# Optimization experiments

Measured on AMD Instinct MI355X. Metric: run time of the kernel, lower is better.

## Reference

```python
import jax, jax.numpy as jnp
import numpy as np

D_MODEL = 256
N_HEADS = 8
WS = 4          # window size
SHIFTED = True
HEAD_DIM = D_MODEL // N_HEADS


def _shift_masks(ws):
    # Masks for the last row / last column of windows after the cyclic shift
    # (standard from-scratch Swin shifted-window mask construction).
    T = ws * ws
    s = ws * (ws // 2)
    row = np.zeros((T, T), np.float32)
    row[-s:, :-s] = -np.inf
    row[:-s, -s:] = -np.inf
    # einops '(r w1) (c w2) -> (w1 r) (w2 c)' with w1=w2=ws
    col = row.reshape(ws, ws, ws, ws).transpose(1, 0, 3, 2).reshape(T, T)
    return jnp.asarray(row), jnp.asarray(col)


def setup_inputs() -> dict:
    key = jax.random.key(0)
    kx, kw, kb = jax.random.split(key, 3)
    x = jax.random.normal(kx, (32, 56 * 56, D_MODEL), jnp.float32)
    W = jax.random.normal(kw, (D_MODEL, 3 * D_MODEL), jnp.float32) * 0.02
    b = jax.random.normal(kb, (3 * D_MODEL,), jnp.float32) * 0.02
    return {"x": x, "W": W, "b": b}


def reference(x, W, b):
    B, L, D = x.shape
    h = w = int(np.sqrt(L))
    ws, nh, hd = WS, N_HEADS, HEAD_DIM
    # QKV projection; torch code splits last dim as (heads, head_dim, 3) -> K innermost
    qkv = (x @ W + b).reshape(B, h, w, nh, hd, 3)
    if SHIFTED:
        qkv = jnp.roll(qkv, (-(ws // 2), -(ws // 2)), axis=(1, 2))
    nwh, nww = h // ws, w // ws
    # window partition: b (i m1) (j m2) n e k -> b n i j (m1 m2) e k
    qkv = qkv.reshape(B, nwh, ws, nww, ws, nh, hd, 3)
    qkv = qkv.transpose(0, 5, 1, 3, 2, 4, 6, 7).reshape(B, nh, nwh, nww, ws * ws, hd, 3)
    q, k, v = qkv[..., 0], qkv[..., 1], qkv[..., 2]
    scores = jnp.einsum('bnijte,bnijse->bnijts', q, k) / jnp.sqrt(jnp.float32(hd))
    if SHIFTED:
        row_mask, col_mask = _shift_masks(ws)
        scores = scores.at[:, :, -1, :].add(row_mask)   # last row of windows
        scores = scores.at[:, :, :, -1].add(col_mask)   # last column of windows
    att = jax.nn.softmax(scores, axis=-1)
    out = jnp.einsum('bnijts,bnijse->bnijte', att, v)
    # reverse window partition: b n i j (m1 m2) e -> b (i m1) (j m2) (n e)
    out = out.reshape(B, nh, nwh, nww, ws, ws, hd)
    out = out.transpose(0, 2, 4, 3, 5, 1, 6).reshape(B, h, w, D)
    if SHIFTED:
        out = jnp.roll(out, (ws // 2, ws // 2), axis=(1, 2))
    return out.reshape(B, L, D)
```

## Files before the change

kernel.cpp:

```cpp
#include <hip/hip_runtime.h>

typedef __attribute__((ext_vector_type(8))) short short8;
typedef __attribute__((ext_vector_type(4))) short short4v;
typedef __attribute__((ext_vector_type(4))) float floatx4;

#define NWSIDE 14
#define HLEN   56
#define DM     256

#define QK_STRIDE 264
#define K_OFF     4224
#define VT_OFF    4224
#define WINB      8448

static __device__ __forceinline__ unsigned int f2bfu(float f) {
    unsigned int u = __float_as_uint(f);
    return (u + 0x7fffu + ((u >> 16) & 1u)) >> 16;
}
static __device__ __forceinline__ unsigned short f2bf(float f) {
    return (unsigned short)f2bfu(f);
}

__global__ void swin_prep(const float* __restrict__ W, const float* __restrict__ bias,
                          unsigned short* __restrict__ Wt, float* __restrict__ bperm) {
    const int k = blockIdx.x;
    const int ks = k >> 5, lq = (k >> 3) & 3, j = k & 7;
    #pragma unroll
    for (int it = 0; it < 3; ++it) {
        const int c = it * 256 + threadIdx.x;
        const float w = W[(size_t)k * 768 + c];
        const int h = c / 96, r = c - h * 96;
        const int e = r / 3, sect = r - e * 3;
        const int cp = h * 96 + sect * 32 + e;
        const int t = cp >> 4, lrow = cp & 15;
        Wt[(size_t)(((t * 8 + ks) * 64 + lq * 16 + lrow) << 3) + j] = f2bf(w);
        if (k == 0) bperm[cp] = bias[c];
    }
}

__global__ __launch_bounds__(256, 4)
void swin_mfma(const float* __restrict__ x,
               const unsigned short* __restrict__ Wt,
               const float* __restrict__ bperm,
               float* __restrict__ out) {
    __shared__ __align__(16) unsigned short lds[2 * WINB];

    const int b    = blockIdx.x / 98;
    const int g    = blockIdx.x % 98;
    const int tid  = threadIdx.x;
    const int wv   = tid >> 6;
    const int lane = tid & 63;
    const int lrow = lane & 15;
    const int lq   = lane >> 4;
    const float scale = 0.17677669529663687f;
    const floatx4 zf = {0.f, 0.f, 0.f, 0.f};

    const int u2 = tid >> 7, tk = (tid >> 3) & 15, sg = tid & 7;
    const int ww2 = g * 2 + u2;
    const int wi2 = ww2 / NWSIDE, wj2 = ww2 % NWSIDE;
    const int gr2 = (wi2 * 4 + (tk >> 2) + 2) % HLEN;
    const int gc2 = (wj2 * 4 + (tk & 3) + 2) % HLEN;
    const size_t rowoff = ((size_t)(b * 3136 + gr2 * 56 + gc2)) * DM;

    {
        const floatx4* xr = (const floatx4*)(x + rowoff);
        unsigned short* xd = &lds[u2 * WINB + tk * QK_STRIDE];
        #pragma unroll
        for (int j = 0; j < 8; ++j) {
            floatx4 f = xr[sg + 8 * j];
            short4v p;
            p[0] = (short)f2bf(f[0]); p[1] = (short)f2bf(f[1]);
            p[2] = (short)f2bf(f[2]); p[3] = (short)f2bf(f[3]);
            *(short4v*)&xd[(sg + 8 * j) * 4] = p;
        }
    }
    __syncthreads();

    const unsigned short* wbase = Wt + (size_t)(96 * wv) * 512 + (size_t)(lane * 8);

    short8 Ab[4];
    #pragma unroll
    for (int f = 0; f < 4; ++f)
        Ab[f] = *(const short8*)(wbase + (f << 9));

    short8 xf[2][8];
    #pragma unroll
    for (int u = 0; u < 2; ++u)
        #pragma unroll
        for (int ks = 0; ks < 8; ++ks)
            xf[u][ks] = *(const short8*)&lds[u * WINB + lrow * QK_STRIDE + ks * 32 + lq * 8];
    __syncthreads();

    floatx4 acc0, acc1, bcv;
    #pragma unroll
    for (int f = 0; f < 64; ++f) {
        const int pi = f >> 3, ks = f & 7;
        if (ks == 0) {
            const int t = 12 * wv + 6 * (pi >> 2) + (pi & 3);
            bcv = *(const floatx4*)&bperm[t * 16 + lq * 4];
            acc0 = zf; acc1 = zf;
        }
        const short8 a = Ab[f & 3];
        if (f + 4 < 64) {
            const int pn = (f + 4) >> 3, kn = (f + 4) & 7;
            Ab[f & 3] = *(const short8*)(wbase + ((48 * (pn >> 2) + 8 * (pn & 3) + kn) << 9));
        }
        acc0 = __builtin_amdgcn_mfma_f32_16x16x32_bf16(a, xf[0][ks], acc0, 0, 0, 0);
        acc1 = __builtin_amdgcn_mfma_f32_16x16x32_bf16(a, xf[1][ks], acc1, 0, 0, 0);
        if (ks == 7) {
            const int h    = 2 * wv + (pi >> 2);
            const int sect = (pi >> 1) & 1;
            const int e0   = (pi & 1) * 16;
            const int base = (sect ? K_OFF : 0) + lrow * QK_STRIDE + h * 32 + e0 + lq * 4;
            short4v p0, p1;
            p0[0] = (short)f2bf(acc0[0] + bcv[0]); p0[1] = (short)f2bf(acc0[1] + bcv[1]);
            p0[2] = (short)f2bf(acc0[2] + bcv[2]); p0[3] = (short)f2bf(acc0[3] + bcv[3]);
            p1[0] = (short)f2bf(acc1[0] + bcv[0]); p1[1] = (short)f2bf(acc1[1] + bcv[1]);
            p1[2] = (short)f2bf(acc1[2] + bcv[2]); p1[3] = (short)f2bf(acc1[3] + bcv[3]);
            *(short4v*)&lds[base]        = p0;
            *(short4v*)&lds[WINB + base] = p1;
        }
    }

    #pragma unroll
    for (int f = 0; f < 4; ++f)
        Ab[f] = *(const short8*)(wbase + ((32 + f) << 9));
    __syncthreads();

    const int u     = wv >> 1;
    const int hbase = (wv & 1) * 4;
    const int ww = g * 2 + u;
    const int wi = ww / NWSIDE, wj = ww % NWSIDE;
    const bool lastrow = (wi == NWSIDE - 1);
    const bool lastcol = (wj == NWSIDE - 1);
    const unsigned short* wl = lds + u * WINB;
    const bool mrow = lastrow && ((lrow >= 8) != (lq >= 2));
    const bool mc   = ((lrow & 3) >= 2);
    const int vtq = (lq & 1) * 8;

    floatx4 ST[4];
    #pragma unroll
    for (int hh = 0; hh < 4; ++hh) {
        const int h = hbase + hh;
        short8 Ak = *(const short8*)&wl[K_OFF + lrow * QK_STRIDE + h * 32 + lq * 8];
        short8 Bq = *(const short8*)&wl[lrow * QK_STRIDE + h * 32 + lq * 8];
        ST[hh] = __builtin_amdgcn_mfma_f32_16x16x32_bf16(Ak, Bq, zf, 0, 0, 0);
    }
    __syncthreads();

    #pragma unroll
    for (int f = 0; f < 32; ++f) {
        const int pi = f >> 3, ks = f & 7;
        if (ks == 0) {
            const int t = 12 * wv + 6 * (pi >> 1) + 4 + (pi & 1);
            bcv = *(const floatx4*)&bperm[t * 16 + lq * 4];
            acc0 = zf; acc1 = zf;
        }
        const short8 a = Ab[f & 3];
        if (f + 4 < 32) {
            const int pn = (f + 4) >> 3, kn = (f + 4) & 7;
            Ab[f & 3] = *(const short8*)(wbase + ((48 * (pn >> 1) + 32 + 8 * (pn & 1) + kn) << 9));
        }
        acc0 = __builtin_amdgcn_mfma_f32_16x16x32_bf16(a, xf[0][ks], acc0, 0, 0, 0);
        acc1 = __builtin_amdgcn_mfma_f32_16x16x32_bf16(a, xf[1][ks], acc1, 0, 0, 0);
        if (ks == 7) {
            const int h  = 2 * wv + (pi >> 1);
            const int e0 = (pi & 1) * 16;
            #pragma unroll
            for (int i = 0; i < 4; ++i) {
                const int rowe = h * 32 + e0 + lq * 4 + i;
                lds[VT_OFF + rowe * 16 + lrow]        = f2bf(acc0[i] + bcv[i]);
                lds[WINB + VT_OFF + rowe * 16 + lrow] = f2bf(acc1[i] + bcv[i]);
            }
        }
    }
    __syncthreads();

    const int gr5 = (wi * 4 + (lrow >> 2) + 2) % HLEN;
    const int gc5 = (wj * 4 + (lrow & 3) + 2) % HLEN;
    float* op = out + ((size_t)(b * 3136 + gr5 * 56 + gc5)) * DM;

    #pragma unroll
    for (int hh = 0; hh < 4; ++hh) {
        const int h = hbase + hh;
        float ev[4];
        #pragma unroll
        for (int i = 0; i < 4; ++i) {
            bool m = mrow || (lastcol && (mc != (i >= 2)));
            ev[i] = __expf(m ? -1e30f : ST[hh][i] * scale);
        }
        float rs = (ev[0] + ev[1]) + (ev[2] + ev[3]);
        rs += __shfl_xor(rs, 16);
        rs += __shfl_xor(rs, 32);
        const float inv = 1.0f / rs;
        const unsigned int d0 = f2bfu(ev[0] * inv) | (f2bfu(ev[1] * inv) << 16);
        const unsigned int d1 = f2bfu(ev[2] * inv) | (f2bfu(ev[3] * inv) << 16);
        const int src0 = lrow + ((lq & 1) << 5);
        int b0 = __shfl((int)d0, src0);
        int b1 = __shfl((int)d1, src0);
        int b2 = __shfl((int)d0, src0 + 16);
        int b3 = __shfl((int)d1, src0 + 16);
        if (lq >= 2) { b0 = 0; b1 = 0; b2 = 0; b3 = 0; }
        union { int i4[4]; short8 s8; } bp;
        bp.i4[0] = b0; bp.i4[1] = b1; bp.i4[2] = b2; bp.i4[3] = b3;
        #pragma unroll
        for (int eb = 0; eb < 2; ++eb) {
            short8 Av = *(const short8*)&wl[VT_OFF + (h * 32 + eb * 16 + lrow) * 16 + vtq];
            floatx4 O = __builtin_amdgcn_mfma_f32_16x16x32_bf16(Av, bp.s8, zf, 0, 0, 0);
            *(floatx4*)&op[h * 32 + eb * 16 + lq * 4] = O;
        }
    }
}

extern "C" void kernel_launch(void* const* d_in, const int* in_sizes, int n_in,
                              void* d_out, int out_size, void* d_ws, size_t ws_size,
                              hipStream_t stream) {
    const float* x    = (const float*)d_in[0];
    const float* W    = (const float*)d_in[1];
    const float* bias = (const float*)d_in[2];
    float* out = (float*)d_out;
    (void)in_sizes; (void)n_in; (void)out_size; (void)ws_size;

    unsigned short* Wt = (unsigned short*)d_ws;
    float* bperm = (float*)((char*)d_ws + 768 * 256 * 2);

    swin_prep<<<256, 256, 0, stream>>>(W, bias, Wt, bperm);
    swin_mfma<<<32 * 98, 256, 0, stream>>>(x, Wt, bperm, out);
}
```

Baseline: 256.9 us.

## Process four windows per block to amortize weight fragment loads across more MFMAs

Each block now handles four windows instead of two, so every weight fragment loaded from global memory feeds four MFMAs instead of two. This halves total weight traffic. The weight prefetch ring grows from four to eight fragments and runs continuously across the Q/K and V projection phases. In the attention phase each wave now handles all eight heads of one window instead of four heads of half a window. The cost is twice the LDS per block, more registers (xf[4][8], acc[4], ST[8]), launch bounds lowered to 2 blocks per CU, and half as many blocks in the grid.

```diff
diff --git a/kernel.cpp b/kernel.cpp
--- a/kernel.cpp
+++ b/kernel.cpp
@@ -19,6 +19,12 @@
 }
 static __device__ __forceinline__ unsigned short f2bf(float f) {
     return (unsigned short)f2bfu(f);
+}
+
+static __device__ __forceinline__ int wfrag_off(int G) {
+    if (G < 64) { const int pi = G >> 3, ks = G & 7; return 48 * (pi >> 2) + 8 * (pi & 3) + ks; }
+    const int Gb = G - 64, pi = Gb >> 3, ks = Gb & 7;
+    return 48 * (pi >> 1) + 32 + 8 * (pi & 1) + ks;
 }
 
 __global__ void swin_prep(const float* __restrict__ W, const float* __restrict__ bias,
@@ -38,15 +44,15 @@
     }
 }
 
-__global__ __launch_bounds__(256, 4)
+__global__ __launch_bounds__(256, 2)
 void swin_mfma(const float* __restrict__ x,
                const unsigned short* __restrict__ Wt,
                const float* __restrict__ bperm,
                float* __restrict__ out) {
-    __shared__ __align__(16) unsigned short lds[2 * WINB];
-
-    const int b    = blockIdx.x / 98;
-    const int g    = blockIdx.x % 98;
+    __shared__ __align__(16) unsigned short lds[4 * WINB];
+
+    const int b    = blockIdx.x / 49;
+    const int g    = blockIdx.x % 49;
     const int tid  = threadIdx.x;
     const int wv   = tid >> 6;
     const int lane = tid & 63;
@@ -55,8 +61,8 @@
     const float scale = 0.17677669529663687f;
     const floatx4 zf = {0.f, 0.f, 0.f, 0.f};
 
-    const int u2 = tid >> 7, tk = (tid >> 3) & 15, sg = tid & 7;
-    const int ww2 = g * 2 + u2;
+    const int tk = lane >> 2, sg = lane & 3;
+    const int ww2 = g * 4 + wv;
     const int wi2 = ww2 / NWSIDE, wj2 = ww2 % NWSIDE;
     const int gr2 = (wi2 * 4 + (tk >> 2) + 2) % HLEN;
     const int gc2 = (wj2 * 4 + (tk & 3) + 2) % HLEN;
@@ -64,87 +70,81 @@
 
     {
         const floatx4* xr = (const floatx4*)(x + rowoff);
-        unsigned short* xd = &lds[u2 * WINB + tk * QK_STRIDE];
-        #pragma unroll
-        for (int j = 0; j < 8; ++j) {
-            floatx4 f = xr[sg + 8 * j];
+        unsigned short* xd = &lds[wv * WINB + tk * QK_STRIDE];
+        #pragma unroll
+        for (int j = 0; j < 16; ++j) {
+            floatx4 f = xr[sg + 4 * j];
             short4v p;
             p[0] = (short)f2bf(f[0]); p[1] = (short)f2bf(f[1]);
             p[2] = (short)f2bf(f[2]); p[3] = (short)f2bf(f[3]);
-            *(short4v*)&xd[(sg + 8 * j) * 4] = p;
+            *(short4v*)&xd[(sg + 4 * j) * 4] = p;
         }
     }
     __syncthreads();
 
     const unsigned short* wbase = Wt + (size_t)(96 * wv) * 512 + (size_t)(lane * 8);
 
-    short8 Ab[4];
-    #pragma unroll
-    for (int f = 0; f < 4; ++f)
-        Ab[f] = *(const short8*)(wbase + (f << 9));
-
-    short8 xf[2][8];
-    #pragma unroll
-    for (int u = 0; u < 2; ++u)
+    short8 Ab[8];
+    #pragma unroll
+    for (int f = 0; f < 8; ++f)
+        Ab[f] = *(const short8*)(wbase + (wfrag_off(f) << 9));
+
+    short8 xf[4][8];
+    #pragma unroll
+    for (int u = 0; u < 4; ++u)
         #pragma unroll
         for (int ks = 0; ks < 8; ++ks)
             xf[u][ks] = *(const short8*)&lds[u * WINB + lrow * QK_STRIDE + ks * 32 + lq * 8];
     __syncthreads();
 
-    floatx4 acc0, acc1, bcv;
+    floatx4 acc[4], bcv;
     #pragma unroll
     for (int f = 0; f < 64; ++f) {
         const int pi = f >> 3, ks = f & 7;
         if (ks == 0) {
             const int t = 12 * wv + 6 * (pi >> 2) + (pi & 3);
             bcv = *(const floatx4*)&bperm[t * 16 + lq * 4];
-            acc0 = zf; acc1 = zf;
-        }
-        const short8 a = Ab[f & 3];
-        if (f + 4 < 64) {
-            const int pn = (f + 4) >> 3, kn = (f + 4) & 7;
-            Ab[f & 3] = *(const short8*)(wbase + ((48 * (pn >> 2) + 8 * (pn & 3) + kn) << 9));
-        }
-        acc0 = __builtin_amdgcn_mfma_f32_16x16x32_bf16(a, xf[0][ks], acc0, 0, 0, 0);
-        acc1 = __builtin_amdgcn_mfma_f32_16x16x32_bf16(a, xf[1][ks], acc1, 0, 0, 0);
+            #pragma unroll
+            for (int u = 0; u < 4; ++u) acc[u] = zf;
+        }
+        const short8 a = Ab[f & 7];
+        Ab[f & 7] = *(const short8*)(wbase + (wfrag_off(f + 8) << 9));
+        #pragma unroll
+        for (int u = 0; u < 4; ++u)
+            acc[u] = __builtin_amdgcn_mfma_f32_16x16x32_bf16(a, xf[u][ks], acc[u], 0, 0, 0);
         if (ks == 7) {
             const int h    = 2 * wv + (pi >> 2);
             const int sect = (pi >> 1) & 1;
             const int e0   = (pi & 1) * 16;
             const int base = (sect ? K_OFF : 0) + lrow * QK_STRIDE + h * 32 + e0 + lq * 4;
-            short4v p0, p1;
-            p0[0] = (short)f2bf(acc0[0] + bcv[0]); p0[1] = (short)f2bf(acc0[1] + bcv[1]);
-            p0[2] = (short)f2bf(acc0[2] + bcv[2]); p0[3] = (short)f2bf(acc0[3] + bcv[3]);
-            p1[0] = (short)f2bf(acc1[0] + bcv[0]); p1[1] = (short)f2bf(acc1[1] + bcv[1]);
-            p1[2] = (short)f2bf(acc1[2] + bcv[2]); p1[3] = (short)f2bf(acc1[3] + bcv[3]);
-            *(short4v*)&lds[base]        = p0;
-            *(short4v*)&lds[WINB + base] = p1;
-        }
-    }
-
-    #pragma unroll
-    for (int f = 0; f < 4; ++f)
-        Ab[f] = *(const short8*)(wbase + ((32 + f) << 9));
-    __syncthreads();
-
-    const int u     = wv >> 1;
-    const int hbase = (wv & 1) * 4;
-    const int ww = g * 2 + u;
+            #pragma unroll
+            for (int u = 0; u < 4; ++u) {
+                short4v p;
+                p[0] = (short)f2bf(acc[u][0] + bcv[0]);
+                p[1] = (short)f2bf(acc[u][1] + bcv[1]);
+                p[2] = (short)f2bf(acc[u][2] + bcv[2]);
+                p[3] = (short)f2bf(acc[u][3] + bcv[3]);
+                *(short4v*)&lds[u * WINB + base] = p;
+            }
+        }
+    }
+    __syncthreads();
+
+    const int ww = g * 4 + wv;
     const int wi = ww / NWSIDE, wj = ww % NWSIDE;
     const bool lastrow = (wi == NWSIDE - 1);
     const bool lastcol = (wj == NWSIDE - 1);
-    const unsigned short* wl = lds + u * WINB;
+    const unsigned short* wl = lds + wv * WINB;
     const bool mrow = lastrow && ((lrow >= 8) != (lq >= 2));
     const bool mc   = ((lrow & 3) >= 2);
     const int vtq = (lq & 1) * 8;
 
-    floatx4 ST[4];
-    #pragma unroll
-    for (int hh = 0; hh < 4; ++hh) {
-        const int h = hbase + hh;
+    floatx4 ST[8];
+    #pragma unroll
+    for (int h = 0; h < 8; ++h) {
         short8 Ak = *(const short8*)&wl[K_OFF + lrow * QK_STRIDE + h * 32 + lq * 8];
         short8 Bq = *(const short8*)&wl[lrow * QK_STRIDE + h * 32 + lq * 8];
-        ST[hh] = __builtin_amdgcn_mfma_f32_16x16x32_bf16(Ak, Bq, zf, 0, 0, 0);
+        ST[h] = __builtin_amdgcn_mfma_f32_16x16x32_bf16(Ak, Bq, zf, 0, 0, 0);
     }
     __syncthreads();
 
@@ -154,24 +154,25 @@
         if (ks == 0) {
             const int t = 12 * wv + 6 * (pi >> 1) + 4 + (pi & 1);
             bcv = *(const floatx4*)&bperm[t * 16 + lq * 4];
-            acc0 = zf; acc1 = zf;
-        }
-        const short8 a = Ab[f & 3];
-        if (f + 4 < 32) {
-            const int pn = (f + 4) >> 3, kn = (f + 4) & 7;
-            Ab[f & 3] = *(const short8*)(wbase + ((48 * (pn >> 1) + 32 + 8 * (pn & 1) + kn) << 9));
-        }
-        acc0 = __builtin_amdgcn_mfma_f32_16x16x32_bf16(a, xf[0][ks], acc0, 0, 0, 0);
-        acc1 = __builtin_amdgcn_mfma_f32_16x16x32_bf16(a, xf[1][ks], acc1, 0, 0, 0);
+            #pragma unroll
+            for (int u = 0; u < 4; ++u) acc[u] = zf;
+        }
+        const short8 a = Ab[f & 7];
+        if (f < 24)
+            Ab[f & 7] = *(const short8*)(wbase + (wfrag_off(72 + f) << 9));
+        #pragma unroll
+        for (int u = 0; u < 4; ++u)
+            acc[u] = __builtin_amdgcn_mfma_f32_16x16x32_bf16(a, xf[u][ks], acc[u], 0, 0, 0);
         if (ks == 7) {
             const int h  = 2 * wv + (pi >> 1);
             const int e0 = (pi & 1) * 16;
             #pragma unroll
-            for (int i = 0; i < 4; ++i) {
-                const int rowe = h * 32 + e0 + lq * 4 + i;
-                lds[VT_OFF + rowe * 16 + lrow]        = f2bf(acc0[i] + bcv[i]);
-                lds[WINB + VT_OFF + rowe * 16 + lrow] = f2bf(acc1[i] + bcv[i]);
-            }
+            for (int u = 0; u < 4; ++u)
+                #pragma unroll
+                for (int i = 0; i < 4; ++i) {
+                    const int rowe = h * 32 + e0 + lq * 4 + i;
+                    lds[u * WINB + VT_OFF + rowe * 16 + lrow] = f2bf(acc[u][i] + bcv[i]);
+                }
         }
     }
     __syncthreads();
@@ -181,13 +182,12 @@
     float* op = out + ((size_t)(b * 3136 + gr5 * 56 + gc5)) * DM;
 
     #pragma unroll
-    for (int hh = 0; hh < 4; ++hh) {
-        const int h = hbase + hh;
+    for (int h = 0; h < 8; ++h) {
         float ev[4];
         #pragma unroll
         for (int i = 0; i < 4; ++i) {
             bool m = mrow || (lastcol && (mc != (i >= 2)));
-            ev[i] = __expf(m ? -1e30f : ST[hh][i] * scale);
+            ev[i] = __expf(m ? -1e30f : ST[h][i] * scale);
         }
         float rs = (ev[0] + ev[1]) + (ev[2] + ev[3]);
         rs += __shfl_xor(rs, 16);
@@ -225,5 +225,5 @@
     float* bperm = (float*)((char*)d_ws + 768 * 256 * 2);
 
     swin_prep<<<256, 256, 0, stream>>>(W, bias, Wt, bperm);
-    swin_mfma<<<32 * 98, 256, 0, stream>>>(x, Wt, bperm, out);
-}
+    swin_mfma<<<32 * 49, 256, 0, stream>>>(x, Wt, bperm, out);
+}
```

Result: faster. 230.7 us (-10.2%).
